# Kernel optimization log

Hardware: AMD Instinct MI355X
Metric: run time of the kernel (lower is better)

Reference implementation:

```python
import jax, jax.numpy as jnp
import numpy as np

B, C, H, W = 32, 3, 128, 128
HID, NP, P, E, NH = 64, 64, 16, 768, 4
MAX_SCALE = 0.3


def conv3x3(x, w, b):
    y = jax.lax.conv_general_dilated(x, w, (1, 1), 'SAME', dimension_numbers=('NCHW', 'OIHW', 'NCHW'))
    return y + b[None, :, None, None]


def mha(t, qkv_w, qkv_b, out_w, out_b):
    # t: (B, T, E) -> standard multi-head self-attention (eval: no dropout)
    b, T, e = t.shape
    dh = e // NH
    qkv = t @ qkv_w.T + qkv_b
    q, k, v = jnp.split(qkv, 3, axis=-1)
    sh = lambda z: z.reshape(b, T, NH, dh).transpose(0, 2, 1, 3)
    q, k, v = sh(q), sh(k), sh(v)
    a = jax.nn.softmax(jnp.einsum('bhqd,bhkd->bhqk', q, k) * np.float32(1.0 / np.sqrt(dh)), axis=-1)
    o = jnp.einsum('bhqk,bhkd->bhqd', a, v).transpose(0, 2, 1, 3).reshape(b, T, e)
    return o @ out_w.T + out_b


def conv_self_attn(x, in_w, in_b, qkv_w, qkv_b, out_w, out_b, proj_w, proj_b):
    # channels are tokens; project spatial dim H*W -> E, attend, project back
    b, c, h, w = x.shape
    t = x.reshape(b, c, h * w) @ in_w.T + in_b
    t = mha(t, qkv_w, qkv_b, out_w, out_b)
    y = t @ proj_w.T + proj_b
    return y.reshape(b, c, h, w)


def maxpool2(x):
    return jax.lax.reduce_window(x, -jnp.inf, jax.lax.max, (1, 1, 2, 2), (1, 1, 2, 2), 'VALID')


def grid_sample_bilinear(img, gx, gy):
    # img: (B,C,H,W); gx,gy: (B,NP,P,P) normalized coords; align_corners=False, zeros padding
    b, c, h, w = img.shape
    xs = ((gx + 1.0) * w - 1.0) * 0.5
    ys = ((gy + 1.0) * h - 1.0) * 0.5
    x0f = jnp.floor(xs); y0f = jnp.floor(ys)
    wx = xs - x0f; wy = ys - y0f
    x0 = x0f.astype(jnp.int32); x1 = x0 + 1
    y0 = y0f.astype(jnp.int32); y1 = y0 + 1
    flat = img.reshape(b, c, h * w)

    def gather(yi, xi):
        valid = (xi >= 0) & (xi < w) & (yi >= 0) & (yi < h)
        idx = jnp.clip(yi, 0, h - 1) * w + jnp.clip(xi, 0, w - 1)
        vals = jax.vmap(lambda f, i: f[:, i])(flat, idx)  # (B,C,NP,P,P)
        return vals * valid[:, None].astype(img.dtype)

    v00 = gather(y0, x0); v01 = gather(y0, x1)
    v10 = gather(y1, x0); v11 = gather(y1, x1)
    wxb = wx[:, None]; wyb = wy[:, None]  # (B,1,NP,P,P)
    out = (v00 * (1 - wxb) * (1 - wyb) + v01 * wxb * (1 - wyb)
           + v10 * (1 - wxb) * wyb + v11 * wxb * wyb)
    return out.transpose(0, 2, 1, 3, 4).reshape(b * NP, c, P, P)


def setup_inputs() -> dict:
    key = jax.random.key(0)
    ks = jax.random.split(key, 32)
    wgt = lambda k, s: jax.random.normal(k, s, dtype=jnp.float32) * 0.02
    HW1, HW2, HC = H * W, (H // 2) * (W // 2), (H // 2) * (W // 2)
    inp = {}
    inp['x'] = jax.random.normal(ks[0], (B, C, H, W), dtype=jnp.float32)
    inp['conv1_w'] = wgt(ks[1], (HID, C, 3, 3)); inp['conv1_b'] = jnp.zeros((HID,), jnp.float32)
    inp['a1_in_w'] = wgt(ks[2], (E, HW1)); inp['a1_in_b'] = jnp.zeros((E,), jnp.float32)
    inp['a1_qkv_w'] = wgt(ks[3], (3 * E, E)); inp['a1_qkv_b'] = jnp.zeros((3 * E,), jnp.float32)
    inp['a1_out_w'] = wgt(ks[4], (E, E)); inp['a1_out_b'] = jnp.zeros((E,), jnp.float32)
    inp['a1_proj_w'] = wgt(ks[5], (HW1, E)); inp['a1_proj_b'] = jnp.zeros((HW1,), jnp.float32)
    inp['conv2_w'] = wgt(ks[6], (NP, HID, 3, 3)); inp['conv2_b'] = jnp.zeros((NP,), jnp.float32)
    inp['a2_in_w'] = wgt(ks[7], (E, HW2)); inp['a2_in_b'] = jnp.zeros((E,), jnp.float32)
    inp['a2_qkv_w'] = wgt(ks[8], (3 * E, E)); inp['a2_qkv_b'] = jnp.zeros((3 * E,), jnp.float32)
    inp['a2_out_w'] = wgt(ks[9], (E, E)); inp['a2_out_b'] = jnp.zeros((E,), jnp.float32)
    inp['a2_proj_w'] = wgt(ks[10], (HW2, E)); inp['a2_proj_b'] = jnp.zeros((HW2,), jnp.float32)
    inp['fc1_w'] = wgt(ks[11], (HC // 2, HC)); inp['fc1_b'] = jnp.zeros((HC // 2,), jnp.float32)
    inp['fc2_w'] = wgt(ks[12], (4, HC // 2)); inp['fc2_b'] = jnp.zeros((4,), jnp.float32)
    return inp


def reference(x, conv1_w, conv1_b, a1_in_w, a1_in_b, a1_qkv_w, a1_qkv_b, a1_out_w, a1_out_b,
              a1_proj_w, a1_proj_b, conv2_w, conv2_b, a2_in_w, a2_in_b, a2_qkv_w, a2_qkv_b,
              a2_out_w, a2_out_b, a2_proj_w, a2_proj_b, fc1_w, fc1_b, fc2_w, fc2_b):
    b = x.shape[0]
    f = jax.nn.relu(conv3x3(x, conv1_w, conv1_b))
    f = conv_self_attn(f, a1_in_w, a1_in_b, a1_qkv_w, a1_qkv_b, a1_out_w, a1_out_b, a1_proj_w, a1_proj_b)
    f = maxpool2(f)
    f = jax.nn.relu(conv3x3(f, conv2_w, conv2_b))
    f = conv_self_attn(f, a2_in_w, a2_in_b, a2_qkv_w, a2_qkv_b, a2_out_w, a2_out_b, a2_proj_w, a2_proj_b)
    feats = f.reshape(b, NP, -1)
    h1 = jax.nn.relu(feats @ fc1_w.T + fc1_b)
    tp = h1 @ fc2_w.T + fc2_b  # (b, NP, 4)
    translate = jnp.tanh(tp[:, :, :2])
    s = jax.nn.sigmoid(tp[:, :, 2:3]) * MAX_SCALE
    sx = s[:, :, 0]; sy = s[:, :, 0]  # isotropic: repeat
    rot = jnp.tanh(tp[:, :, 3]) * np.float32(np.pi)
    cos = jnp.cos(rot); sin = jnp.sin(rot)
    x_ext = jnp.minimum(sx * jnp.abs(cos) + sy * jnp.abs(sin), 1.0)
    y_ext = jnp.minimum(sx * jnp.abs(sin) + sy * jnp.abs(cos), 1.0)
    translate = translate * (1.0 - jnp.stack([x_ext, y_ext], axis=-1))
    ta = sx * cos; tb_ = -sx * sin; tc = sy * sin; td = sy * cos
    tx = translate[:, :, 0]; ty = translate[:, :, 1]
    base = (2.0 * jnp.arange(P, dtype=jnp.float32) + 1.0) / P - 1.0  # align_corners=False grid
    gx = ta[..., None, None] * base[None, None, None, :] + tb_[..., None, None] * base[None, None, :, None] + tx[..., None, None]
    gy = tc[..., None, None] * base[None, None, None, :] + td[..., None, None] * base[None, None, :, None] + ty[..., None, None]
    patches = grid_sample_bilinear(x, gx, gy)  # (B*NP, C, P, P)
    return (patches, translate)
```

## Files before the change

### kernel.cpp

```cpp
#include <hip/hip_runtime.h>
#include <hip/hip_bf16.h>
#include <math.h>


#define PI_F 3.14159265358979323846f

typedef float f32x4 __attribute__((ext_vector_type(4)));
typedef short short8 __attribute__((ext_vector_type(8)));
typedef unsigned short us4 __attribute__((ext_vector_type(4)));
typedef __hip_bfloat16 bf16;

__device__ __forceinline__ void async16(const void* g, void* l) {
  __builtin_amdgcn_global_load_lds(
      (const __attribute__((address_space(1))) void*)g,
      (__attribute__((address_space(3))) void*)l, 16, 0, 0);
}

template <int MODE>
__global__ __launch_bounds__(256) void gemm_bf16(
    const unsigned short* __restrict__ A, const unsigned short* __restrict__ Bw,
    const float* __restrict__ bias, void* __restrict__ Cout,
    int M, int N, int K, int kchunk) {
  __shared__ unsigned short As[128 * 32];
  __shared__ unsigned short Bs[128 * 32];
  const int tid = threadIdx.x;
  const int bmT = M >> 7, bnT = N >> 7;
  int l = blockIdx.x;
  const int gsize = 8 * bnT;
  int gid = l / gsize;
  int rem = l - gid * gsize;
  int fm = gid * 8;
  int gsz = bmT - fm; if (gsz > 8) gsz = 8;
  const int bm = (fm + rem % gsz) << 7;
  const int bn = (rem / gsz) << 7;
  const int k0 = blockIdx.z * kchunk;
  const int wave = tid >> 6;
  const int lane = tid & 63;
  const int wm = (wave & 1) << 6, wn = (wave >> 1) << 6;
  const int r0 = tid >> 2;
  const int c0 = (tid & 3) << 3;
  const unsigned short* Ag0 = A + (size_t)(bm + r0) * K + k0 + c0;
  const unsigned short* Ag1 = Ag0 + (size_t)64 * K;
  const unsigned short* Bg0 = Bw + (size_t)(bn + r0) * K + k0 + c0;
  const unsigned short* Bg1 = Bg0 + (size_t)64 * K;
  unsigned short* Al = As + wave * 512;
  unsigned short* Bl = Bs + wave * 512;
  f32x4 acc[4][4] = {};
  const int fr = lane & 15;
  const int fk = (lane >> 4) << 3;
  for (int kt = 0; kt < kchunk; kt += 32) {
    async16(Ag0 + kt, Al);
    async16(Ag1 + kt, Al + 2048);
    async16(Bg0 + kt, Bl);
    async16(Bg1 + kt, Bl + 2048);
    __syncthreads();
    short8 af[4], bf[4];
    #pragma unroll
    for (int i = 0; i < 4; ++i)
      af[i] = *(const short8*)(As + ((wm + i * 16 + fr) << 5) + fk);
    #pragma unroll
    for (int i = 0; i < 4; ++i)
      bf[i] = *(const short8*)(Bs + ((wn + i * 16 + fr) << 5) + fk);
    #pragma unroll
    for (int mi = 0; mi < 4; ++mi)
      #pragma unroll
      for (int ni = 0; ni < 4; ++ni)
        acc[mi][ni] = __builtin_amdgcn_mfma_f32_16x16x32_bf16(af[mi], bf[ni], acc[mi][ni], 0, 0, 0);
    __syncthreads();
  }
  const int cr = (lane >> 4) << 2;
  const int cc = lane & 15;
  if (MODE == 0) {
    float* C = (float*)Cout + (size_t)blockIdx.z * M * N;
    #pragma unroll
    for (int mi = 0; mi < 4; ++mi)
      #pragma unroll
      for (int ni = 0; ni < 4; ++ni) {
        int col = bn + wn + ni * 16 + cc;
        #pragma unroll
        for (int r = 0; r < 4; ++r)
          C[(size_t)(bm + wm + mi * 16 + cr + r) * N + col] = acc[mi][ni][r];
      }
  } else {
    #pragma unroll
    for (int ni = 0; ni < 4; ++ni) {
      int col = bn + wn + ni * 16 + cc;
      float bv = bias[col];
      #pragma unroll
      for (int mi = 0; mi < 4; ++mi)
        #pragma unroll
        for (int r = 0; r < 4; ++r) {
          size_t idx = (size_t)(bm + wm + mi * 16 + cr + r) * N + col;
          float v = acc[mi][ni][r] + bv;
          if (MODE == 1) ((float*)Cout)[idx] = v;
          else ((bf16*)Cout)[idx] = __float2bfloat16(v);
        }
    }
  }
}

__global__ __launch_bounds__(256) void reduce_bias_k(
    const float* __restrict__ part, const float* __restrict__ bias,
    bf16* __restrict__ out, int MN, int N, int S, int relu) {
  int i = blockIdx.x * 256 + threadIdx.x;
  if (i >= (MN >> 2)) return;
  float4 s = ((const float4*)part)[i];
  for (int z = 1; z < S; ++z) {
    float4 q = *(const float4*)(part + (size_t)z * MN + i * 4);
    s.x += q.x; s.y += q.y; s.z += q.z; s.w += q.w;
  }
  int nb = (i * 4) % N;
  float4 bv = *(const float4*)(bias + nb);
  s.x += bv.x; s.y += bv.y; s.z += bv.z; s.w += bv.w;
  if (relu) {
    s.x = fmaxf(s.x, 0.f); s.y = fmaxf(s.y, 0.f);
    s.z = fmaxf(s.z, 0.f); s.w = fmaxf(s.w, 0.f);
  }
  bf16 vals[4] = {__float2bfloat16(s.x), __float2bfloat16(s.y),
                  __float2bfloat16(s.z), __float2bfloat16(s.w)};
  *(us4*)(out + (size_t)i * 4) = *(const us4*)vals;
}

__global__ __launch_bounds__(256) void cvt3_k(
    const float* __restrict__ s0, bf16* __restrict__ d0, int n0,
    const float* __restrict__ s1, bf16* __restrict__ d1, int n1,
    const float* __restrict__ s2, bf16* __restrict__ d2, int n2) {
  int i = blockIdx.x * 256 + threadIdx.x;
  const float* s; bf16* d; int j = i;
  if (j < n0) { s = s0; d = d0; }
  else {
    j -= n0;
    if (j < n1) { s = s1; d = d1; }
    else { j -= n1; if (j >= n2) return; s = s2; d = d2; }
  }
  float4 v = ((const float4*)s)[j];
  bf16 vals[4] = {__float2bfloat16(v.x), __float2bfloat16(v.y),
                  __float2bfloat16(v.z), __float2bfloat16(v.w)};
  *(us4*)(d + (size_t)j * 4) = *(const us4*)vals;
}

__global__ __launch_bounds__(256) void cvt_wcl_k(
    const float* __restrict__ w, bf16* __restrict__ wcl) {
  int i = blockIdx.x * 256 + threadIdx.x;
  if (i >= 36864) return;
  int ic = i & 63, oc = (i >> 6) & 63, s = i >> 12;
  wcl[i] = __float2bfloat16(w[oc * 576 + ic * 9 + s]);
}

__global__ __launch_bounds__(256) void conv3x3_relu_c3_fast(
    const float* __restrict__ x, const float* __restrict__ w,
    const float* __restrict__ bias, bf16* __restrict__ out) {
  __shared__ float xs[3][4][132];
  __shared__ float wsm[3][9][64];
  const int tid = threadIdx.x;
  const int b = blockIdx.y;
  const int y0 = blockIdx.x * 2;
  const int xg = (tid & 15) * 8;
  const int row = (tid >> 4) & 1;
  const int oc0 = (tid >> 5) * 8;
  for (int i = tid; i < 3 * 4 * 132; i += 256) {
    int c = i % 132;
    int r = (i / 132) % 4;
    int ic = i / (132 * 4);
    int gy = y0 + r - 1;
    int gx = c - 1;
    float v = 0.f;
    if ((unsigned)gy < 128u && (unsigned)gx < 128u)
      v = x[((size_t)(b * 3 + ic) << 14) + gy * 128 + gx];
    xs[ic][r][c] = v;
  }
  for (int i = tid; i < 3 * 9 * 64; i += 256) {
    int oc = i & 63;
    int k = (i >> 6) % 9;
    int ic = i / (64 * 9);
    wsm[ic][k][oc] = w[oc * 27 + ic * 9 + k];
  }
  __syncthreads();
  float acc[8][8] = {};
  #pragma unroll
  for (int ic = 0; ic < 3; ++ic) {
    #pragma unroll
    for (int ky = 0; ky < 3; ++ky) {
      const float* rp = &xs[ic][row + ky][xg];
      float4 r0 = *(const float4*)(rp);
      float4 r1 = *(const float4*)(rp + 4);
      float4 r2 = *(const float4*)(rp + 8);
      float v[10] = {r0.x, r0.y, r0.z, r0.w, r1.x, r1.y, r1.z, r1.w, r2.x, r2.y};
      #pragma unroll
      for (int kx = 0; kx < 3; ++kx) {
        const float* wr = &wsm[ic][ky * 3 + kx][oc0];
        float4 w0 = *(const float4*)(wr);
        float4 w1 = *(const float4*)(wr + 4);
        float wv[8] = {w0.x, w0.y, w0.z, w0.w, w1.x, w1.y, w1.z, w1.w};
        #pragma unroll
        for (int o = 0; o < 8; ++o)
          #pragma unroll
          for (int p = 0; p < 8; ++p)
            acc[o][p] += wv[o] * v[p + kx];
      }
    }
  }
  #pragma unroll
  for (int o = 0; o < 8; ++o) {
    float bo = bias[oc0 + o];
    bf16 vals[8];
    #pragma unroll
    for (int p = 0; p < 8; ++p) vals[p] = __float2bfloat16(fmaxf(acc[o][p] + bo, 0.f));
    bf16* op = out + ((size_t)(b * 64 + oc0 + o) << 14) + (y0 + row) * 128 + xg;
    *(uint4*)op = *(const uint4*)vals;
  }
}

__global__ __launch_bounds__(256) void maxpool_cl(
    const bf16* __restrict__ y1, bf16* __restrict__ xp) {
  int wave = threadIdx.x >> 6;
  int lane = threadIdx.x & 63;
  int cell = blockIdx.x * 4 + wave;
  int b = blockIdx.y;
  int yp = cell / 66, xq = cell % 66;
  bf16* dst = xp + (((size_t)b * 66 + yp) * 66 + xq) * 64 + lane;
  if (yp == 0 || yp == 65 || xq == 0 || xq == 65) {
    *dst = __float2bfloat16(0.f);
    return;
  }
  int py = yp - 1, px = xq - 1;
  const bf16* sp = y1 + ((size_t)(b * 64 + lane) << 14) + (py * 2) * 128 + px * 2;
  float a = __bfloat162float(sp[0]), bq = __bfloat162float(sp[1]);
  float c = __bfloat162float(sp[128]), d = __bfloat162float(sp[129]);
  *dst = __float2bfloat16(fmaxf(fmaxf(a, bq), fmaxf(c, d)));
}

__global__ __launch_bounds__(256) void conv2_mfma(
    const bf16* __restrict__ xp, const bf16* __restrict__ wcl,
    const float* __restrict__ bias, bf16* __restrict__ f3) {
  __shared__ unsigned short As[128 * 32];
  __shared__ unsigned short Bs[64 * 32];
  const int tid = threadIdx.x;
  const int b = blockIdx.y;
  const int y0 = blockIdx.x * 2;
  const int wave = tid >> 6;
  const int lane = tid & 63;
  const int wm = (wave & 1) << 6;
  const int wn = (wave >> 1) << 5;
  const char* xpB = (const char*)(xp + (size_t)b * 66 * 66 * 64);
  const char* wclB = (const char*)wcl;
  const int sr = tid >> 2;
  const int soff = (tid & 3) << 4;
  unsigned short* Al = As + wave * 512;
  unsigned short* Bl = Bs + wave * 512;
  f32x4 acc[4][2] = {};
  const int fr = lane & 15;
  const int fk = (lane >> 4) << 3;
  for (int tap = 0; tap < 9; ++tap) {
    int dy = tap / 3, dx = tap % 3;
    const char* arow0 = xpB + (((y0 + dy) * 66 + dx) << 7);
    const char* brow = wclB + (tap << 13);
    #pragma unroll
    for (int ch = 0; ch < 2; ++ch) {
      int coff = (ch << 6) + soff;
      async16(arow0 + sr * 128 + coff, Al);
      async16(arow0 + 66 * 128 + sr * 128 + coff, Al + 2048);
      async16(brow + sr * 128 + coff, Bl);
      __syncthreads();
      short8 af[4], bf[2];
      #pragma unroll
      for (int i = 0; i < 4; ++i)
        af[i] = *(const short8*)(As + ((wm + i * 16 + fr) << 5) + fk);
      #pragma unroll
      for (int i = 0; i < 2; ++i)
        bf[i] = *(const short8*)(Bs + ((wn + i * 16 + fr) << 5) + fk);
      #pragma unroll
      for (int mi = 0; mi < 4; ++mi)
        #pragma unroll
        for (int ni = 0; ni < 2; ++ni)
          acc[mi][ni] = __builtin_amdgcn_mfma_f32_16x16x32_bf16(af[mi], bf[ni], acc[mi][ni], 0, 0, 0);
      __syncthreads();
    }
  }
  const int cr = (lane >> 4) << 2;
  const int cc = lane & 15;
  #pragma unroll
  for (int ni = 0; ni < 2; ++ni) {
    int oc = wn + ni * 16 + cc;
    float bv = bias[oc];
    #pragma unroll
    for (int mi = 0; mi < 4; ++mi) {
      int pxb = wm + mi * 16 + cr;
      int y = y0 + (pxb >> 6), xb = pxb & 63;
      bf16 vals[4];
      #pragma unroll
      for (int r = 0; r < 4; ++r)
        vals[r] = __float2bfloat16(fmaxf(acc[mi][ni][r] + bv, 0.f));
      bf16* op = f3 + (((size_t)(b * 64 + oc)) << 12) + y * 64 + xb;
      *(us4*)op = *(const us4*)vals;
    }
  }
}

__global__ __launch_bounds__(256) void attn_fused(
    const bf16* __restrict__ qkv, bf16* __restrict__ o, float scale) {
  __shared__ unsigned short Qs[64][216];
  __shared__ unsigned short Ks[64][216];
  __shared__ unsigned short Vt[192][72];
  __shared__ unsigned short Ps[64][72];
  const int tid = threadIdx.x;
  const int b = blockIdx.x >> 2, h = blockIdx.x & 3;
  const unsigned short* base = (const unsigned short*)qkv + (size_t)b * 64 * 2304 + h * 192;
  for (int c = tid; c < 1536; c += 256) {
    int tok = c / 24, idx = (c % 24) * 8;
    const unsigned short* rp = base + (size_t)tok * 2304 + idx;
    short8 qv = *(const short8*)(rp);
    short8 kv = *(const short8*)(rp + 768);
    short8 vv = *(const short8*)(rp + 1536);
    *(short8*)&Qs[tok][idx] = qv;
    *(short8*)&Ks[tok][idx] = kv;
    #pragma unroll
    for (int j = 0; j < 8; ++j) Vt[idx + j][tok] = (unsigned short)vv[j];
  }
  __syncthreads();
  const int wave = tid >> 6, lane = tid & 63;
  const int fr = lane & 15;
  const int fk = (lane >> 4) << 3;
  f32x4 accs[4] = {};
  #pragma unroll
  for (int kk = 0; kk < 6; ++kk) {
    short8 aq = *(const short8*)&Qs[wave * 16 + fr][kk * 32 + fk];
    #pragma unroll
    for (int n = 0; n < 4; ++n) {
      short8 bk = *(const short8*)&Ks[n * 16 + fr][kk * 32 + fk];
      accs[n] = __builtin_amdgcn_mfma_f32_16x16x32_bf16(aq, bk, accs[n], 0, 0, 0);
    }
  }
  const int cr = (lane >> 4) << 2;
  const int cc = lane & 15;
  #pragma unroll
  for (int r = 0; r < 4; ++r) {
    float v0 = accs[0][r] * scale, v1 = accs[1][r] * scale;
    float v2 = accs[2][r] * scale, v3 = accs[3][r] * scale;
    float m = fmaxf(fmaxf(v0, v1), fmaxf(v2, v3));
    #pragma unroll
    for (int off = 8; off; off >>= 1) m = fmaxf(m, __shfl_xor(m, off));
    float e0 = __expf(v0 - m), e1 = __expf(v1 - m);
    float e2 = __expf(v2 - m), e3 = __expf(v3 - m);
    float s = e0 + e1 + e2 + e3;
    #pragma unroll
    for (int off = 8; off; off >>= 1) s += __shfl_xor(s, off);
    float inv = 1.f / s;
    int q = wave * 16 + cr + r;
    Ps[q][0 * 16 + cc] = __bfloat16_as_ushort(__float2bfloat16(e0 * inv));
    Ps[q][1 * 16 + cc] = __bfloat16_as_ushort(__float2bfloat16(e1 * inv));
    Ps[q][2 * 16 + cc] = __bfloat16_as_ushort(__float2bfloat16(e2 * inv));
    Ps[q][3 * 16 + cc] = __bfloat16_as_ushort(__float2bfloat16(e3 * inv));
  }
  __syncthreads();
  f32x4 acco[12] = {};
  #pragma unroll
  for (int kk = 0; kk < 2; ++kk) {
    short8 ap = *(const short8*)&Ps[wave * 16 + fr][kk * 32 + fk];
    #pragma unroll
    for (int j = 0; j < 12; ++j) {
      short8 bv = *(const short8*)&Vt[j * 16 + fr][kk * 32 + fk];
      acco[j] = __builtin_amdgcn_mfma_f32_16x16x32_bf16(ap, bv, acco[j], 0, 0, 0);
    }
  }
  bf16* ob = o + (size_t)(b * 64) * 768 + h * 192;
  #pragma unroll
  for (int j = 0; j < 12; ++j) {
    int d = j * 16 + cc;
    #pragma unroll
    for (int r = 0; r < 4; ++r) {
      int q = wave * 16 + cr + r;
      ob[(size_t)q * 768 + d] = __float2bfloat16(acco[j][r]);
    }
  }
}

__global__ __launch_bounds__(256) void fc2_wave(
    const bf16* __restrict__ A, const float* __restrict__ Bw,
    const float* __restrict__ bias, float* __restrict__ C, int K) {
  int m = blockIdx.x;
  int n = threadIdx.x >> 6;
  int lane = threadIdx.x & 63;
  const bf16* a = A + (size_t)m * K;
  const float* bb = Bw + (size_t)n * K;
  float acc = 0.f;
  for (int k = lane; k < K; k += 64)
    acc += __bfloat162float(a[k]) * bb[k];
  for (int off = 32; off; off >>= 1) acc += __shfl_xor(acc, off);
  if (lane == 0) C[m * 4 + n] = acc + bias[n];
}

__global__ __launch_bounds__(64) void params_k(
    const float* __restrict__ tp, float* __restrict__ par, float* __restrict__ trans_out) {
  int m = blockIdx.x * 64 + threadIdx.x;
  if (m >= 2048) return;
  float t0 = tp[m * 4 + 0], t1 = tp[m * 4 + 1], t2 = tp[m * 4 + 2], t3 = tp[m * 4 + 3];
  float trx = tanhf(t0), tryy = tanhf(t1);
  float s = (1.f / (1.f + expf(-t2))) * 0.3f;
  float rot = tanhf(t3) * PI_F;
  float c = cosf(rot), sn = sinf(rot);
  float x_ext = fminf(s * fabsf(c) + s * fabsf(sn), 1.f);
  float y_ext = fminf(s * fabsf(sn) + s * fabsf(c), 1.f);
  float tx = trx * (1.f - x_ext);
  float ty = tryy * (1.f - y_ext);
  par[m * 8 + 0] = s * c;
  par[m * 8 + 1] = -s * sn;
  par[m * 8 + 2] = s * sn;
  par[m * 8 + 3] = s * c;
  par[m * 8 + 4] = tx;
  par[m * 8 + 5] = ty;
  trans_out[m * 2 + 0] = tx;
  trans_out[m * 2 + 1] = ty;
}

__global__ __launch_bounds__(256) void sample_k(
    const float* __restrict__ x, const float* __restrict__ par, float* __restrict__ out) {
  int tid = blockIdx.x * 256 + threadIdx.x;
  if (tid >= 32 * 64 * 3 * 256) return;
  int pj = tid & 15, pi = (tid >> 4) & 15;
  int c = (tid >> 8) % 3;
  int bp = tid / 768;
  int b = bp >> 6;
  const float* pp = par + bp * 8;
  float ta = pp[0], tb = pp[1], tc = pp[2], td = pp[3], tx = pp[4], ty = pp[5];
  float bj = (2.f * pj + 1.f) / 16.f - 1.f;
  float bi = (2.f * pi + 1.f) / 16.f - 1.f;
  float gx = ta * bj + tb * bi + tx;
  float gy = tc * bj + td * bi + ty;
  float xs = ((gx + 1.f) * 128.f - 1.f) * 0.5f;
  float ys = ((gy + 1.f) * 128.f - 1.f) * 0.5f;
  float x0f = floorf(xs), y0f = floorf(ys);
  float wx = xs - x0f, wy = ys - y0f;
  int x0 = (int)x0f, y0 = (int)y0f, x1 = x0 + 1, y1 = y0 + 1;
  const float* img = x + ((size_t)b * 3 + c) * 16384;
  auto g = [&](int yi, int xi) -> float {
    bool v = (xi >= 0) && (xi < 128) && (yi >= 0) && (yi < 128);
    int yc = yi < 0 ? 0 : (yi > 127 ? 127 : yi);
    int xc = xi < 0 ? 0 : (xi > 127 ? 127 : xi);
    float val = img[yc * 128 + xc];
    return v ? val : 0.f;
  };
  float v00 = g(y0, x0), v01 = g(y0, x1), v10 = g(y1, x0), v11 = g(y1, x1);
  out[tid] = v00 * (1.f - wx) * (1.f - wy) + v01 * wx * (1.f - wy) +
             v10 * (1.f - wx) * wy + v11 * wx * wy;
}

extern "C" void kernel_launch(void* const* d_in, const int* in_sizes, int n_in,
                              void* d_out, int out_size, void* d_ws, size_t ws_size,
                              hipStream_t stream) {
  const float* x        = (const float*)d_in[0];
  const float* conv1_w  = (const float*)d_in[1];
  const float* conv1_b  = (const float*)d_in[2];
  const float* a1_in_w  = (const float*)d_in[3];
  const float* a1_in_b  = (const float*)d_in[4];
  const float* a1_qkv_w = (const float*)d_in[5];
  const float* a1_qkv_b = (const float*)d_in[6];
  const float* a1_out_w = (const float*)d_in[7];
  const float* a1_out_b = (const float*)d_in[8];
  const float* a1_proj_w = (const float*)d_in[9];
  const float* a1_proj_b = (const float*)d_in[10];
  const float* conv2_w  = (const float*)d_in[11];
  const float* conv2_b  = (const float*)d_in[12];
  const float* a2_in_w  = (const float*)d_in[13];
  const float* a2_in_b  = (const float*)d_in[14];
  const float* a2_qkv_w = (const float*)d_in[15];
  const float* a2_qkv_b = (const float*)d_in[16];
  const float* a2_out_w = (const float*)d_in[17];
  const float* a2_out_b = (const float*)d_in[18];
  const float* a2_proj_w = (const float*)d_in[19];
  const float* a2_proj_b = (const float*)d_in[20];
  const float* fc1_w    = (const float*)d_in[21];
  const float* fc1_b    = (const float*)d_in[22];
  const float* fc2_w    = (const float*)d_in[23];
  const float* fc2_b    = (const float*)d_in[24];
  float* out = (float*)d_out;

  char* ws = (char*)d_ws;
  bf16*  f1   = (bf16*)(ws + 0);
  bf16*  y1   = f1;
  bf16*  f3   = (bf16*)(ws + 0);
  bf16*  h1   = (bf16*)(ws + 33554432);
  float* part = (float*)(ws + 83886080);
  bf16*  xp   = (bf16*)(ws + 83886080);
  bf16*  t    = (bf16*)(ws + 134217728);
  bf16*  qkv  = (bf16*)(ws + 137363456);
  bf16*  o    = (bf16*)(ws + 158334976);
  bf16*  ao   = (bf16*)(ws + 161480704);
  bf16*  y2   = (bf16*)(ws + 164626432);
  float* tp   = (float*)(ws + 181403648);
  float* par  = (float*)(ws + 181436416);
  bf16*  W    = (bf16*)(ws + 181501952);
  bf16*  wcl  = W;
  bf16*  Wq   = (bf16*)(ws + 164626432);
  bf16*  Wo   = (bf16*)(ws + 164626432 + 3538944);

  const unsigned short* Wu = (const unsigned short*)W;
  const unsigned short* Wqu = (const unsigned short*)Wq;
  const unsigned short* Wou = (const unsigned short*)Wo;
  const float scale = 0.07216878364870323f;

  const int n_in1 = 768 * 16384 / 4, n_qkv = 2304 * 768 / 4, n_out = 768 * 768 / 4;
  const int n_in2 = 768 * 4096 / 4;
  const int n_proj1 = 16384 * 768 / 4, n_proj2 = 4096 * 768 / 4, n_fc1 = 2048 * 4096 / 4;

  conv3x3_relu_c3_fast<<<dim3(64, 32), 256, 0, stream>>>(x, conv1_w, conv1_b, f1);
  cvt3_k<<<(n_in1 + n_qkv + n_out + 255) / 256, 256, 0, stream>>>(
      a1_in_w, W, n_in1, a1_qkv_w, Wq, n_qkv, a1_out_w, Wo, n_out);
  gemm_bf16<0><<<dim3(96, 1, 8), 256, 0, stream>>>((const unsigned short*)f1, Wu, nullptr, part, 2048, 768, 16384, 2048);
  reduce_bias_k<<<1536, 256, 0, stream>>>(part, a1_in_b, t, 2048 * 768, 768, 8, 0);
  gemm_bf16<2><<<dim3(288, 1, 1), 256, 0, stream>>>((const unsigned short*)t, Wqu, a1_qkv_b, qkv, 2048, 2304, 768, 768);
  attn_fused<<<128, 256, 0, stream>>>(qkv, o, scale);
  gemm_bf16<0><<<dim3(96, 1, 3), 256, 0, stream>>>((const unsigned short*)o, Wou, nullptr, part, 2048, 768, 768, 256);
  reduce_bias_k<<<1536, 256, 0, stream>>>(part, a1_out_b, ao, 2048 * 768, 768, 3, 0);
  cvt3_k<<<(n_proj1 + 255) / 256, 256, 0, stream>>>(
      a1_proj_w, W, n_proj1, nullptr, nullptr, 0, nullptr, nullptr, 0);
  gemm_bf16<2><<<dim3(2048, 1, 1), 256, 0, stream>>>((const unsigned short*)ao, Wu, a1_proj_b, y1, 2048, 16384, 768, 768);
  cvt_wcl_k<<<144, 256, 0, stream>>>(conv2_w, wcl);
  maxpool_cl<<<dim3(1089, 32), 256, 0, stream>>>(y1, xp);
  conv2_mfma<<<dim3(32, 32), 256, 0, stream>>>(xp, wcl, conv2_b, f3);
  cvt3_k<<<(n_in2 + n_qkv + n_out + 255) / 256, 256, 0, stream>>>(
      a2_in_w, W, n_in2, a2_qkv_w, Wq, n_qkv, a2_out_w, Wo, n_out);
  gemm_bf16<0><<<dim3(96, 1, 4), 256, 0, stream>>>((const unsigned short*)f3, Wu, nullptr, part, 2048, 768, 4096, 1024);
  reduce_bias_k<<<1536, 256, 0, stream>>>(part, a2_in_b, t, 2048 * 768, 768, 4, 0);
  gemm_bf16<2><<<dim3(288, 1, 1), 256, 0, stream>>>((const unsigned short*)t, Wqu, a2_qkv_b, qkv, 2048, 2304, 768, 768);
  attn_fused<<<128, 256, 0, stream>>>(qkv, o, scale);
  gemm_bf16<0><<<dim3(96, 1, 3), 256, 0, stream>>>((const unsigned short*)o, Wou, nullptr, part, 2048, 768, 768, 256);
  reduce_bias_k<<<1536, 256, 0, stream>>>(part, a2_out_b, ao, 2048 * 768, 768, 3, 0);
  cvt3_k<<<(n_proj2 + 255) / 256, 256, 0, stream>>>(
      a2_proj_w, W, n_proj2, nullptr, nullptr, 0, nullptr, nullptr, 0);
  gemm_bf16<2><<<dim3(512, 1, 1), 256, 0, stream>>>((const unsigned short*)ao, Wu, a2_proj_b, y2, 2048, 4096, 768, 768);
  cvt3_k<<<(n_fc1 + 255) / 256, 256, 0, stream>>>(
      fc1_w, W, n_fc1, nullptr, nullptr, 0, nullptr, nullptr, 0);
  gemm_bf16<0><<<dim3(256, 1, 2), 256, 0, stream>>>((const unsigned short*)y2, Wu, nullptr, part, 2048, 2048, 4096, 2048);
  reduce_bias_k<<<4096, 256, 0, stream>>>(part, fc1_b, h1, 2048 * 2048, 2048, 2, 1);
  fc2_wave<<<2048, 256, 0, stream>>>(h1, fc2_w, fc2_b, tp, 2048);
  params_k<<<32, 64, 0, stream>>>(tp, par, out + 1572864);
  sample_k<<<6144, 256, 0, stream>>>(x, par, out);
}
```

Measured before the change: 773.7 us.

## Fuse fp32 weight conversion into GEMM B-tile loads and merge fc2 with params

The separate fp32-to-bf16 weight conversion kernels are removed. The GEMM now loads fp32 weight tiles into registers, converts them, and stores them to LDS, which avoids writing and re-reading converted weight buffers. The split-K index moves from blockIdx.z into a flattened blockIdx.x. fc2 and the parameter kernel are merged into one launch. The trade-off is that B loads become synchronous register loads of twice the bytes instead of async LDS loads, and weights reused across M tiles are converted repeatedly.

```diff
diff --git a/kernel.cpp b/kernel.cpp
--- a/kernel.cpp
+++ b/kernel.cpp
@@ -16,16 +16,25 @@
       (__attribute__((address_space(3))) void*)l, 16, 0, 0);
 }
 
-template <int MODE>
+__device__ __forceinline__ short8 f8_to_bf8(float4 a, float4 b) {
+  bf16 v[8] = {__float2bfloat16(a.x), __float2bfloat16(a.y),
+               __float2bfloat16(a.z), __float2bfloat16(a.w),
+               __float2bfloat16(b.x), __float2bfloat16(b.y),
+               __float2bfloat16(b.z), __float2bfloat16(b.w)};
+  return *(const short8*)v;
+}
+
+template <int MODE, int S>
 __global__ __launch_bounds__(256) void gemm_bf16(
-    const unsigned short* __restrict__ A, const unsigned short* __restrict__ Bw,
+    const unsigned short* __restrict__ A, const float* __restrict__ Bw,
     const float* __restrict__ bias, void* __restrict__ Cout,
     int M, int N, int K, int kchunk) {
   __shared__ unsigned short As[128 * 32];
   __shared__ unsigned short Bs[128 * 32];
   const int tid = threadIdx.x;
+  const int idz = (S > 1) ? (blockIdx.x % S) : 0;
+  int l = (S > 1) ? (blockIdx.x / S) : blockIdx.x;
   const int bmT = M >> 7, bnT = N >> 7;
-  int l = blockIdx.x;
   const int gsize = 8 * bnT;
   int gid = l / gsize;
   int rem = l - gid * gsize;
@@ -33,7 +42,7 @@
   int gsz = bmT - fm; if (gsz > 8) gsz = 8;
   const int bm = (fm + rem % gsz) << 7;
   const int bn = (rem / gsz) << 7;
-  const int k0 = blockIdx.z * kchunk;
+  const int k0 = idz * kchunk;
   const int wave = tid >> 6;
   const int lane = tid & 63;
   const int wm = (wave & 1) << 6, wn = (wave >> 1) << 6;
@@ -41,18 +50,21 @@
   const int c0 = (tid & 3) << 3;
   const unsigned short* Ag0 = A + (size_t)(bm + r0) * K + k0 + c0;
   const unsigned short* Ag1 = Ag0 + (size_t)64 * K;
-  const unsigned short* Bg0 = Bw + (size_t)(bn + r0) * K + k0 + c0;
-  const unsigned short* Bg1 = Bg0 + (size_t)64 * K;
+  const float* Bf0 = Bw + (size_t)(bn + r0) * K + k0 + c0;
+  const float* Bf1 = Bf0 + (size_t)64 * K;
   unsigned short* Al = As + wave * 512;
-  unsigned short* Bl = Bs + wave * 512;
   f32x4 acc[4][4] = {};
   const int fr = lane & 15;
   const int fk = (lane >> 4) << 3;
   for (int kt = 0; kt < kchunk; kt += 32) {
+    float4 b0a = *(const float4*)(Bf0 + kt);
+    float4 b0b = *(const float4*)(Bf0 + kt + 4);
+    float4 b1a = *(const float4*)(Bf1 + kt);
+    float4 b1b = *(const float4*)(Bf1 + kt + 4);
     async16(Ag0 + kt, Al);
     async16(Ag1 + kt, Al + 2048);
-    async16(Bg0 + kt, Bl);
-    async16(Bg1 + kt, Bl + 2048);
+    *(short8*)(Bs + (tid << 3)) = f8_to_bf8(b0a, b0b);
+    *(short8*)(Bs + (tid << 3) + 2048) = f8_to_bf8(b1a, b1b);
     __syncthreads();
     short8 af[4], bf[4];
     #pragma unroll
@@ -71,7 +83,7 @@
   const int cr = (lane >> 4) << 2;
   const int cc = lane & 15;
   if (MODE == 0) {
-    float* C = (float*)Cout + (size_t)blockIdx.z * M * N;
+    float* C = (float*)Cout + (size_t)idz * M * N;
     #pragma unroll
     for (int mi = 0; mi < 4; ++mi)
       #pragma unroll
@@ -91,9 +103,7 @@
         #pragma unroll
         for (int r = 0; r < 4; ++r) {
           size_t idx = (size_t)(bm + wm + mi * 16 + cr + r) * N + col;
-          float v = acc[mi][ni][r] + bv;
-          if (MODE == 1) ((float*)Cout)[idx] = v;
-          else ((bf16*)Cout)[idx] = __float2bfloat16(v);
+          ((bf16*)Cout)[idx] = __float2bfloat16(acc[mi][ni][r] + bv);
         }
     }
   }
@@ -119,24 +129,6 @@
   bf16 vals[4] = {__float2bfloat16(s.x), __float2bfloat16(s.y),
                   __float2bfloat16(s.z), __float2bfloat16(s.w)};
   *(us4*)(out + (size_t)i * 4) = *(const us4*)vals;
-}
-
-__global__ __launch_bounds__(256) void cvt3_k(
-    const float* __restrict__ s0, bf16* __restrict__ d0, int n0,
-    const float* __restrict__ s1, bf16* __restrict__ d1, int n1,
-    const float* __restrict__ s2, bf16* __restrict__ d2, int n2) {
-  int i = blockIdx.x * 256 + threadIdx.x;
-  const float* s; bf16* d; int j = i;
-  if (j < n0) { s = s0; d = d0; }
-  else {
-    j -= n0;
-    if (j < n1) { s = s1; d = d1; }
-    else { j -= n1; if (j >= n2) return; s = s2; d = d2; }
-  }
-  float4 v = ((const float4*)s)[j];
-  bf16 vals[4] = {__float2bfloat16(v.x), __float2bfloat16(v.y),
-                  __float2bfloat16(v.z), __float2bfloat16(v.w)};
-  *(us4*)(d + (size_t)j * 4) = *(const us4*)vals;
 }
 
 __global__ __launch_bounds__(256) void cvt_wcl_k(
@@ -375,9 +367,11 @@
   }
 }
 
-__global__ __launch_bounds__(256) void fc2_wave(
+__global__ __launch_bounds__(256) void fc2_params(
     const bf16* __restrict__ A, const float* __restrict__ Bw,
-    const float* __restrict__ bias, float* __restrict__ C, int K) {
+    const float* __restrict__ bias, float* __restrict__ par,
+    float* __restrict__ trans_out, int K) {
+  __shared__ float sm[4];
   int m = blockIdx.x;
   int n = threadIdx.x >> 6;
   int lane = threadIdx.x & 63;
@@ -387,30 +381,27 @@
   for (int k = lane; k < K; k += 64)
     acc += __bfloat162float(a[k]) * bb[k];
   for (int off = 32; off; off >>= 1) acc += __shfl_xor(acc, off);
-  if (lane == 0) C[m * 4 + n] = acc + bias[n];
-}
-
-__global__ __launch_bounds__(64) void params_k(
-    const float* __restrict__ tp, float* __restrict__ par, float* __restrict__ trans_out) {
-  int m = blockIdx.x * 64 + threadIdx.x;
-  if (m >= 2048) return;
-  float t0 = tp[m * 4 + 0], t1 = tp[m * 4 + 1], t2 = tp[m * 4 + 2], t3 = tp[m * 4 + 3];
-  float trx = tanhf(t0), tryy = tanhf(t1);
-  float s = (1.f / (1.f + expf(-t2))) * 0.3f;
-  float rot = tanhf(t3) * PI_F;
-  float c = cosf(rot), sn = sinf(rot);
-  float x_ext = fminf(s * fabsf(c) + s * fabsf(sn), 1.f);
-  float y_ext = fminf(s * fabsf(sn) + s * fabsf(c), 1.f);
-  float tx = trx * (1.f - x_ext);
-  float ty = tryy * (1.f - y_ext);
-  par[m * 8 + 0] = s * c;
-  par[m * 8 + 1] = -s * sn;
-  par[m * 8 + 2] = s * sn;
-  par[m * 8 + 3] = s * c;
-  par[m * 8 + 4] = tx;
-  par[m * 8 + 5] = ty;
-  trans_out[m * 2 + 0] = tx;
-  trans_out[m * 2 + 1] = ty;
+  if (lane == 0) sm[n] = acc + bias[n];
+  __syncthreads();
+  if (threadIdx.x == 0) {
+    float t0 = sm[0], t1 = sm[1], t2 = sm[2], t3 = sm[3];
+    float trx = tanhf(t0), tryy = tanhf(t1);
+    float s = (1.f / (1.f + expf(-t2))) * 0.3f;
+    float rot = tanhf(t3) * PI_F;
+    float c = cosf(rot), sn = sinf(rot);
+    float x_ext = fminf(s * fabsf(c) + s * fabsf(sn), 1.f);
+    float y_ext = fminf(s * fabsf(sn) + s * fabsf(c), 1.f);
+    float tx = trx * (1.f - x_ext);
+    float ty = tryy * (1.f - y_ext);
+    par[m * 8 + 0] = s * c;
+    par[m * 8 + 1] = -s * sn;
+    par[m * 8 + 2] = s * sn;
+    par[m * 8 + 3] = s * c;
+    par[m * 8 + 4] = tx;
+    par[m * 8 + 5] = ty;
+    trans_out[m * 2 + 0] = tx;
+    trans_out[m * 2 + 1] = ty;
+  }
 }
 
 __global__ __launch_bounds__(256) void sample_k(
@@ -487,53 +478,31 @@
   bf16*  o    = (bf16*)(ws + 158334976);
   bf16*  ao   = (bf16*)(ws + 161480704);
   bf16*  y2   = (bf16*)(ws + 164626432);
-  float* tp   = (float*)(ws + 181403648);
   float* par  = (float*)(ws + 181436416);
-  bf16*  W    = (bf16*)(ws + 181501952);
-  bf16*  wcl  = W;
-  bf16*  Wq   = (bf16*)(ws + 164626432);
-  bf16*  Wo   = (bf16*)(ws + 164626432 + 3538944);
-
-  const unsigned short* Wu = (const unsigned short*)W;
-  const unsigned short* Wqu = (const unsigned short*)Wq;
-  const unsigned short* Wou = (const unsigned short*)Wo;
+  bf16*  wcl  = (bf16*)(ws + 181501952);
+
   const float scale = 0.07216878364870323f;
 
-  const int n_in1 = 768 * 16384 / 4, n_qkv = 2304 * 768 / 4, n_out = 768 * 768 / 4;
-  const int n_in2 = 768 * 4096 / 4;
-  const int n_proj1 = 16384 * 768 / 4, n_proj2 = 4096 * 768 / 4, n_fc1 = 2048 * 4096 / 4;
-
   conv3x3_relu_c3_fast<<<dim3(64, 32), 256, 0, stream>>>(x, conv1_w, conv1_b, f1);
-  cvt3_k<<<(n_in1 + n_qkv + n_out + 255) / 256, 256, 0, stream>>>(
-      a1_in_w, W, n_in1, a1_qkv_w, Wq, n_qkv, a1_out_w, Wo, n_out);
-  gemm_bf16<0><<<dim3(96, 1, 8), 256, 0, stream>>>((const unsigned short*)f1, Wu, nullptr, part, 2048, 768, 16384, 2048);
+  gemm_bf16<0, 8><<<96 * 8, 256, 0, stream>>>((const unsigned short*)f1, a1_in_w, nullptr, part, 2048, 768, 16384, 2048);
   reduce_bias_k<<<1536, 256, 0, stream>>>(part, a1_in_b, t, 2048 * 768, 768, 8, 0);
-  gemm_bf16<2><<<dim3(288, 1, 1), 256, 0, stream>>>((const unsigned short*)t, Wqu, a1_qkv_b, qkv, 2048, 2304, 768, 768);
+  gemm_bf16<2, 1><<<288, 256, 0, stream>>>((const unsigned short*)t, a1_qkv_w, a1_qkv_b, qkv, 2048, 2304, 768, 768);
   attn_fused<<<128, 256, 0, stream>>>(qkv, o, scale);
-  gemm_bf16<0><<<dim3(96, 1, 3), 256, 0, stream>>>((const unsigned short*)o, Wou, nullptr, part, 2048, 768, 768, 256);
+  gemm_bf16<0, 3><<<96 * 3, 256, 0, stream>>>((const unsigned short*)o, a1_out_w, nullptr, part, 2048, 768, 768, 256);
   reduce_bias_k<<<1536, 256, 0, stream>>>(part, a1_out_b, ao, 2048 * 768, 768, 3, 0);
-  cvt3_k<<<(n_proj1 + 255) / 256, 256, 0, stream>>>(
-      a1_proj_w, W, n_proj1, nullptr, nullptr, 0, nullptr, nullptr, 0);
-  gemm_bf16<2><<<dim3(2048, 1, 1), 256, 0, stream>>>((const unsigned short*)ao, Wu, a1_proj_b, y1, 2048, 16384, 768, 768);
+  gemm_bf16<2, 1><<<2048, 256, 0, stream>>>((const unsigned short*)ao, a1_proj_w, a1_proj_b, y1, 2048, 16384, 768, 768);
   cvt_wcl_k<<<144, 256, 0, stream>>>(conv2_w, wcl);
   maxpool_cl<<<dim3(1089, 32), 256, 0, stream>>>(y1, xp);
   conv2_mfma<<<dim3(32, 32), 256, 0, stream>>>(xp, wcl, conv2_b, f3);
-  cvt3_k<<<(n_in2 + n_qkv + n_out + 255) / 256, 256, 0, stream>>>(
-      a2_in_w, W, n_in2, a2_qkv_w, Wq, n_qkv, a2_out_w, Wo, n_out);
-  gemm_bf16<0><<<dim3(96, 1, 4), 256, 0, stream>>>((const unsigned short*)f3, Wu, nullptr, part, 2048, 768, 4096, 1024);
+  gemm_bf16<0, 4><<<96 * 4, 256, 0, stream>>>((const unsigned short*)f3, a2_in_w, nullptr, part, 2048, 768, 4096, 1024);
   reduce_bias_k<<<1536, 256, 0, stream>>>(part, a2_in_b, t, 2048 * 768, 768, 4, 0);
-  gemm_bf16<2><<<dim3(288, 1, 1), 256, 0, stream>>>((const unsigned short*)t, Wqu, a2_qkv_b, qkv, 2048, 2304, 768, 768);
+  gemm_bf16<2, 1><<<288, 256, 0, stream>>>((const unsigned short*)t, a2_qkv_w, a2_qkv_b, qkv, 2048, 2304, 768, 768);
   attn_fused<<<128, 256, 0, stream>>>(qkv, o, scale);
-  gemm_bf16<0><<<dim3(96, 1, 3), 256, 0, stream>>>((const unsigned short*)o, Wou, nullptr, part, 2048, 768, 768, 256);
+  gemm_bf16<0, 3><<<96 * 3, 256, 0, stream>>>((const unsigned short*)o, a2_out_w, nullptr, part, 2048, 768, 768, 256);
   reduce_bias_k<<<1536, 256, 0, stream>>>(part, a2_out_b, ao, 2048 * 768, 768, 3, 0);
-  cvt3_k<<<(n_proj2 + 255) / 256, 256, 0, stream>>>(
-      a2_proj_w, W, n_proj2, nullptr, nullptr, 0, nullptr, nullptr, 0);
-  gemm_bf16<2><<<dim3(512, 1, 1), 256, 0, stream>>>((const unsigned short*)ao, Wu, a2_proj_b, y2, 2048, 4096, 768, 768);
-  cvt3_k<<<(n_fc1 + 255) / 256, 256, 0, stream>>>(
-      fc1_w, W, n_fc1, nullptr, nullptr, 0, nullptr, nullptr, 0);
-  gemm_bf16<0><<<dim3(256, 1, 2), 256, 0, stream>>>((const unsigned short*)y2, Wu, nullptr, part, 2048, 2048, 4096, 2048);
+  gemm_bf16<2, 1><<<512, 256, 0, stream>>>((const unsigned short*)ao, a2_proj_w, a2_proj_b, y2, 2048, 4096, 768, 768);
+  gemm_bf16<0, 2><<<256 * 2, 256, 0, stream>>>((const unsigned short*)y2, fc1_w, nullptr, part, 2048, 2048, 4096, 2048);
   reduce_bias_k<<<4096, 256, 0, stream>>>(part, fc1_b, h1, 2048 * 2048, 2048, 2, 1);
-  fc2_wave<<<2048, 256, 0, stream>>>(h1, fc2_w, fc2_b, tp, 2048);
-  params_k<<<32, 64, 0, stream>>>(tp, par, out + 1572864);
+  fc2_params<<<2048, 256, 0, stream>>>(h1, fc2_w, fc2_b, par, out + 1572864, 2048);
   sample_k<<<6144, 256, 0, stream>>>(x, par, out);
 }
```

Result: slower. 879.2 us (+13.6%).
